# Kernel optimization log

Measured on AMD Instinct MI355X. Metric: run time of the kernel, lower is better.

## Reference

```python
import jax, jax.numpy as jnp
import numpy as np

B, N, D, NHOP = 16, 1024, 128, 4


def setup_inputs() -> dict:
    key = jax.random.key(0)
    ks = jax.random.split(key, 7)
    x = jax.random.normal(ks[0], (B, N, D), jnp.float32)
    # sparse symmetric binary adjacency with self loops (adj>0 masking semantics)
    a = (jax.random.uniform(ks[1], (B, N, N)) < 0.05).astype(jnp.float32)
    adj = jnp.maximum(a, a.transpose(0, 2, 1))
    adj = jnp.maximum(adj, jnp.eye(N, dtype=jnp.float32))
    s = 1.0 / np.sqrt(D)
    W_w = jax.random.normal(ks[2], (D, D), jnp.float32) * s
    W_b = jax.random.normal(ks[3], (D,), jnp.float32) * 0.01
    A = jax.random.normal(ks[4], (D, D), jnp.float32) * s
    gate_w = jax.random.normal(ks[5], (1, 2 * D), jnp.float32) * (1.0 / np.sqrt(2 * D))
    gate_b = jax.random.normal(ks[6], (1,), jnp.float32) * 0.01
    return {"x": x, "adj": adj, "W_w": W_w, "W_b": W_b, "A": A,
            "gate_w": gate_w, "gate_b": gate_b}


def reference(x, adj, W_w, W_b, A, gate_w, gate_b):
    # h = W(x)                                  [B,N,D]
    h = jnp.einsum('bnf,df->bnd', x, W_w) + W_b
    # bilinear attention scores e_ij = (hA)_i . h_j, symmetrized
    hA = jnp.einsum('bnd,de->bne', h, A)        # [B,N,D]
    e = jnp.einsum('bjl,bkl->bjk', hA, h)       # [B,N,N]
    e = e + e.transpose(0, 2, 1)
    att = jnp.where(adj > 0, e, jnp.zeros((), e.dtype))
    att = jax.nn.softmax(att, axis=1)           # softmax over dim=1 as in torch
    att = att * adj
    z = h
    for _ in range(NHOP):
        az = jax.nn.relu(jnp.einsum('bij,bjk->bik', att, z))   # [B,N,D]
        g_in = jnp.concatenate([x, az], axis=-1)               # [B,N,2D]
        coeff = jax.nn.sigmoid(jnp.einsum('bnf,of->bno', g_in, gate_w) + gate_b)  # [B,N,1]
        z = coeff * x + (1.0 - coeff) * az
    return z
```

## Files before the change

kernel.cpp:

```cpp
#include <hip/hip_runtime.h>
#include <cstdint>
#include <cstddef>

#define BB 16
#define NN 1024
#define DD 128
#define RR (BB*NN)
#define MAXDEG 256
#define NHOP 4

typedef unsigned long long u64;
typedef unsigned short u16;
typedef unsigned int u32;

__global__ void k_compact(const float* __restrict__ adj,
                          u64* __restrict__ bm, u32* __restrict__ deg) {
  int row = blockIdx.x;
  int l = threadIdx.x;
  const float* arow = adj + (size_t)row * NN;
  int base = 0;
  for (int r = 0; r < 16; ++r) {
    float v = arow[r * 64 + l];
    u64 m = __ballot(v > 0.0f);
    if (l == 0) bm[row * 16 + r] = m;
    base += __popcll(m);
  }
  if (l == 0) deg[row] = (u32)base;
}

__global__ void k_transpose(const float* __restrict__ A, float* __restrict__ At) {
  int e = blockIdx.x * 256 + threadIdx.x;
  int r = e >> 7, c = e & 127;
  At[c * 128 + r] = A[r * 128 + c];
}

#define GB_BK 64
__global__ __launch_bounds__(256, 3)
void k_gemm_bt(const float* __restrict__ Am, const float* __restrict__ Bm,
               const float* __restrict__ bias, float* __restrict__ Cm) {
  __shared__ float a_lds[64][GB_BK + 1];
  __shared__ float b_lds[128][GB_BK + 1];
  int t = threadIdx.x;
  int tj = t >> 5;
  int tk = t & 31;
  int rowbase = blockIdx.x * 64;
  float acc[8][4];
#pragma unroll
  for (int i = 0; i < 8; i++)
#pragma unroll
    for (int j = 0; j < 4; j++) acc[i][j] = 0.f;

  for (int kc = 0; kc < 128; kc += GB_BK) {
#pragma unroll
    for (int i = 0; i < 4; ++i) {
      int e = t + i * 256;
      int r = e >> 4, kq = e & 15;
      float4 v = *(const float4*)(Am + (size_t)(rowbase + r) * DD + kc + kq * 4);
      a_lds[r][kq * 4 + 0] = v.x; a_lds[r][kq * 4 + 1] = v.y;
      a_lds[r][kq * 4 + 2] = v.z; a_lds[r][kq * 4 + 3] = v.w;
    }
#pragma unroll
    for (int i = 0; i < 8; ++i) {
      int e = t + i * 256;
      int r = e >> 4, kq = e & 15;
      float4 v = *(const float4*)(Bm + (size_t)r * DD + kc + kq * 4);
      b_lds[r][kq * 4 + 0] = v.x; b_lds[r][kq * 4 + 1] = v.y;
      b_lds[r][kq * 4 + 2] = v.z; b_lds[r][kq * 4 + 3] = v.w;
    }
    __syncthreads();
#pragma unroll
    for (int kk = 0; kk < GB_BK; ++kk) {
      float av[8], bv[4];
#pragma unroll
      for (int i = 0; i < 8; i++) av[i] = a_lds[tj + 8 * i][kk];
#pragma unroll
      for (int j = 0; j < 4; j++) bv[j] = b_lds[tk + 32 * j][kk];
#pragma unroll
      for (int i = 0; i < 8; i++)
#pragma unroll
        for (int j = 0; j < 4; j++)
          acc[i][j] = fmaf(av[i], bv[j], acc[i][j]);
    }
    __syncthreads();
  }
#pragma unroll
  for (int i = 0; i < 8; i++) {
    int gr = rowbase + tj + 8 * i;
#pragma unroll
    for (int j = 0; j < 4; j++) {
      int c = tk + 32 * j;
      float v = acc[i][j];
      if (bias) v += bias[c];
      Cm[(size_t)gr * DD + c] = v;
    }
  }
}

#define EB_BK 32
__global__ __launch_bounds__(256, 2)
void k_e(const float* __restrict__ h, const float* __restrict__ hA,
         const u64* __restrict__ bm, float* __restrict__ ep) {
  extern __shared__ float smem[];
  float* haj = smem;
  float* hj  = smem + 128 * 33;
  float* hak = smem + 2 * 128 * 33;
  float* hk  = smem + 3 * 128 * 33;

  int pid = blockIdx.x;
  int b = blockIdx.y;
  int Jt = 0;
  while (pid >= 8 - Jt) { pid -= (8 - Jt); Jt++; }
  int Kt = Jt + pid;

  int t = threadIdx.x;
  int tj = t >> 4;
  int tk = t & 15;
  const float* hb  = h  + (size_t)b * NN * DD;
  const float* hAb = hA + (size_t)b * NN * DD;

  float acc[8][8];
#pragma unroll
  for (int i = 0; i < 8; i++)
#pragma unroll
    for (int j = 0; j < 8; j++) acc[i][j] = 0.f;

  for (int kc = 0; kc < 128; kc += EB_BK) {
#pragma unroll
    for (int i = 0; i < 4; ++i) {
      int e = t + i * 256;
      int r = e >> 3, kq = e & 7;
      float4 v;
      v = *(const float4*)(hAb + (size_t)(Jt * 128 + r) * DD + kc + kq * 4);
      haj[r * 33 + kq * 4 + 0] = v.x; haj[r * 33 + kq * 4 + 1] = v.y;
      haj[r * 33 + kq * 4 + 2] = v.z; haj[r * 33 + kq * 4 + 3] = v.w;
      v = *(const float4*)(hb + (size_t)(Jt * 128 + r) * DD + kc + kq * 4);
      hj[r * 33 + kq * 4 + 0] = v.x; hj[r * 33 + kq * 4 + 1] = v.y;
      hj[r * 33 + kq * 4 + 2] = v.z; hj[r * 33 + kq * 4 + 3] = v.w;
      v = *(const float4*)(hAb + (size_t)(Kt * 128 + r) * DD + kc + kq * 4);
      hak[r * 33 + kq * 4 + 0] = v.x; hak[r * 33 + kq * 4 + 1] = v.y;
      hak[r * 33 + kq * 4 + 2] = v.z; hak[r * 33 + kq * 4 + 3] = v.w;
      v = *(const float4*)(hb + (size_t)(Kt * 128 + r) * DD + kc + kq * 4);
      hk[r * 33 + kq * 4 + 0] = v.x; hk[r * 33 + kq * 4 + 1] = v.y;
      hk[r * 33 + kq * 4 + 2] = v.z; hk[r * 33 + kq * 4 + 3] = v.w;
    }
    __syncthreads();
#pragma unroll
    for (int kk = 0; kk < EB_BK; ++kk) {
      float aJ[8], bK[8], aK[8], bJ[8];
#pragma unroll
      for (int i = 0; i < 8; i++) { aJ[i] = haj[(tj + 16 * i) * 33 + kk]; bJ[i] = hj[(tj + 16 * i) * 33 + kk]; }
#pragma unroll
      for (int j = 0; j < 8; j++) { bK[j] = hk[(tk + 16 * j) * 33 + kk]; aK[j] = hak[(tk + 16 * j) * 33 + kk]; }
#pragma unroll
      for (int i = 0; i < 8; i++)
#pragma unroll
        for (int j = 0; j < 8; j++)
          acc[i][j] = fmaf(aJ[i], bK[j], fmaf(aK[j], bJ[i], acc[i][j]));
    }
    __syncthreads();
  }

#pragma unroll
  for (int i = 0; i < 8; i++) {
    int jr = Jt * 128 + tj + 16 * i;
    u64 w0 = bm[((size_t)b * NN + jr) * 16 + 2 * Kt];
    u64 w1 = bm[((size_t)b * NN + jr) * 16 + 2 * Kt + 1];
#pragma unroll
    for (int j = 0; j < 8; j++) {
      int kc2 = tk + 16 * j;
      int kcg = Kt * 128 + kc2;
      u64 w = (kc2 < 64) ? w0 : w1;
      int bit = (int)((w >> (kc2 & 63)) & 1ull);
      float v = bit ? acc[i][j] : 0.f;
      ep[((size_t)b * NN + jr) * NN + kcg] = v;
      ep[((size_t)b * NN + kcg) * NN + jr] = v;
    }
  }
}

__global__ void k_stats(const float* __restrict__ ep,
                        float* __restrict__ mrow, float* __restrict__ rden) {
  int row = blockIdx.x * 4 + (threadIdx.x >> 6);
  int l = threadIdx.x & 63;
  const float* er = ep + (size_t)row * NN;
  float v[16];
  float mx = -INFINITY;
#pragma unroll
  for (int r = 0; r < 16; r++) { v[r] = er[r * 64 + l]; mx = fmaxf(mx, v[r]); }
#pragma unroll
  for (int s = 1; s < 64; s <<= 1) mx = fmaxf(mx, __shfl_xor(mx, s, 64));
  float sum = 0.f;
#pragma unroll
  for (int r = 0; r < 16; r++) sum += __expf(v[r] - mx);
#pragma unroll
  for (int s = 1; s < 64; s <<= 1) sum += __shfl_xor(sum, s, 64);
  if (l == 0) { mrow[row] = mx; rden[row] = 1.0f / sum; }
}

__global__ void k_att(const float* __restrict__ ep, const u64* __restrict__ bm,
                      const float* __restrict__ mrow, const float* __restrict__ rden,
                      float* __restrict__ attv, u16* __restrict__ idx) {
  int row = blockIdx.x * 4 + (threadIdx.x >> 6);
  int l = threadIdx.x & 63;
  int bbase = row & ~(NN - 1);
  const float* er = ep + (size_t)row * NN;
  float* av = attv + (size_t)row * MAXDEG;
  u16* ir = idx + (size_t)row * MAXDEG;
  int base = 0;
  for (int r = 0; r < 16; r++) {
    u64 w = bm[row * 16 + r];
    int k = r * 64 + l;
    float v = er[k];
    if ((w >> l) & 1ull) {
      float a = __expf(v - mrow[bbase + k]) * rden[bbase + k];
      int pos = base + __popcll(w & ((1ull << l) - 1ull));
      if (pos < MAXDEG) { av[pos] = a; ir[pos] = (u16)k; }
    }
    base += __popcll(w);
  }
}

__global__ __launch_bounds__(256, 1)
void k_az(const float* __restrict__ z, const float* __restrict__ attv,
          const u16* __restrict__ idx, const u32* __restrict__ deg,
          float* __restrict__ az) {
  extern __shared__ float zl[];
  int b = blockIdx.x, kt = blockIdx.y, rc = blockIdx.z;
  int c0 = kt * 32;
  int t = threadIdx.x;
  const float* zb = z + (size_t)b * NN * DD;
#pragma unroll 8
  for (int i = 0; i < 32; i++) {
    int e = t + i * 256;
    int q = e >> 3, cq = e & 7;
    float4 v = *(const float4*)(zb + (size_t)q * DD + c0 + cq * 4);
    *(float4*)(zl + q * 36 + cq * 4) = v;
  }
  __syncthreads();

  int grow = b * NN + rc * 256 + t;
  int dgi = (int)deg[grow]; if (dgi > MAXDEG) dgi = MAXDEG;
  const u16* ir = idx + (size_t)grow * MAXDEG;
  const float* ar = attv + (size_t)grow * MAXDEG;

  float acc[32];
#pragma unroll
  for (int c = 0; c < 32; c++) acc[c] = 0.f;

  int s = 0;
  ushort4 q4 = {0, 0, 0, 0};
  float4 a4 = {0.f, 0.f, 0.f, 0.f};
  if (s + 4 <= dgi) { q4 = *(const ushort4*)(ir); a4 = *(const float4*)(ar); }
  for (; s + 4 <= dgi; s += 4) {
    ushort4 cq = q4; float4 ca = a4;
    if (s + 8 <= dgi) { q4 = *(const ushort4*)(ir + s + 4); a4 = *(const float4*)(ar + s + 4); }
    const unsigned short qq[4] = {cq.x, cq.y, cq.z, cq.w};
    const float aa[4] = {ca.x, ca.y, ca.z, ca.w};
#pragma unroll
    for (int e = 0; e < 4; e++) {
      const float* zr = zl + (int)qq[e] * 36;
      float a = aa[e];
#pragma unroll
      for (int cc = 0; cc < 8; cc++) {
        float4 zv = *(const float4*)(zr + cc * 4);
        acc[cc * 4 + 0] = fmaf(a, zv.x, acc[cc * 4 + 0]);
        acc[cc * 4 + 1] = fmaf(a, zv.y, acc[cc * 4 + 1]);
        acc[cc * 4 + 2] = fmaf(a, zv.z, acc[cc * 4 + 2]);
        acc[cc * 4 + 3] = fmaf(a, zv.w, acc[cc * 4 + 3]);
      }
    }
  }
  for (; s < dgi; s++) {
    int q = ir[s];
    float a = ar[s];
    const float* zr = zl + q * 36;
#pragma unroll
    for (int cc = 0; cc < 8; cc++) {
      float4 zv = *(const float4*)(zr + cc * 4);
      acc[cc * 4 + 0] = fmaf(a, zv.x, acc[cc * 4 + 0]);
      acc[cc * 4 + 1] = fmaf(a, zv.y, acc[cc * 4 + 1]);
      acc[cc * 4 + 2] = fmaf(a, zv.z, acc[cc * 4 + 2]);
      acc[cc * 4 + 3] = fmaf(a, zv.w, acc[cc * 4 + 3]);
    }
  }

  float* ao = az + (size_t)grow * DD + c0;
#pragma unroll
  for (int c = 0; c < 32; c += 4) {
    float4 v;
    v.x = fmaxf(acc[c + 0], 0.f); v.y = fmaxf(acc[c + 1], 0.f);
    v.z = fmaxf(acc[c + 2], 0.f); v.w = fmaxf(acc[c + 3], 0.f);
    *(float4*)(ao + c) = v;
  }
}

__global__ void k_gate(const float* __restrict__ x, const float* __restrict__ az,
                       const float* __restrict__ gw, const float* __restrict__ gb,
                       float* __restrict__ zo) {
  int row = blockIdx.x * 4 + (threadIdx.x >> 6);
  int l = threadIdx.x & 63;
  const float* xr = x + (size_t)row * DD;
  const float* ar = az + (size_t)row * DD;
  float x0 = xr[l], x1 = xr[l + 64];
  float a0 = ar[l], a1 = ar[l + 64];
  float p = gw[l] * x0 + gw[l + 64] * x1 + gw[128 + l] * a0 + gw[192 + l] * a1;
#pragma unroll
  for (int s = 1; s < 64; s <<= 1) p += __shfl_xor(p, s, 64);
  float cf = 1.0f / (1.0f + __expf(-(p + gb[0])));
  zo[(size_t)row * DD + l] = cf * x0 + (1.f - cf) * a0;
  zo[(size_t)row * DD + l + 64] = cf * x1 + (1.f - cf) * a1;
}

extern "C" void kernel_launch(void* const* d_in, const int* in_sizes, int n_in,
                              void* d_out, int out_size, void* d_ws, size_t ws_size,
                              hipStream_t stream) {
  const float* x   = (const float*)d_in[0];
  const float* adj = (const float*)d_in[1];
  const float* W_w = (const float*)d_in[2];
  const float* W_b = (const float*)d_in[3];
  const float* A   = (const float*)d_in[4];
  const float* gw  = (const float*)d_in[5];
  const float* gb  = (const float*)d_in[6];
  float* out = (float*)d_out;

  char* p = (char*)d_ws;
  auto alloc = [&](size_t bytes) -> void* {
    void* r = (void*)p;
    p += (bytes + 255) & ~(size_t)255;
    return r;
  };
  float* h    = (float*)alloc((size_t)RR * DD * 4);
  float* hA   = (float*)alloc((size_t)RR * DD * 4);
  float* ep   = (float*)alloc((size_t)RR * NN * 4);
  u64*   bm   = (u64*)alloc((size_t)RR * 16 * 8);
  u32*   deg  = (u32*)alloc((size_t)RR * 4);
  float* mrow = (float*)alloc((size_t)RR * 4);
  float* rden = (float*)alloc((size_t)RR * 4);
  float* attv = (float*)alloc((size_t)RR * MAXDEG * 4);
  u16*   idx  = (u16*)alloc((size_t)RR * MAXDEG * 2);
  float* At   = (float*)alloc((size_t)DD * DD * 4);

  k_compact<<<RR, 64, 0, stream>>>(adj, bm, deg);
  k_transpose<<<64, 256, 0, stream>>>(A, At);
  k_gemm_bt<<<RR / 64, 256, 0, stream>>>(x, W_w, W_b, h);
  k_gemm_bt<<<RR / 64, 256, 0, stream>>>(h, At, nullptr, hA);
  size_t e_lds = (size_t)4 * 128 * 33 * sizeof(float);
  k_e<<<dim3(36, 16), 256, e_lds, stream>>>(h, hA, bm, ep);
  k_stats<<<RR / 4, 256, 0, stream>>>(ep, mrow, rden);
  k_att<<<RR / 4, 256, 0, stream>>>(ep, bm, mrow, rden, attv, idx);

  size_t az_lds = (size_t)1024 * 36 * sizeof(float);
  for (int hop = 0; hop < NHOP; ++hop) {
    k_az<<<dim3(16, 4, 4), 256, az_lds, stream>>>(h, attv, idx, deg, hA);
    float* zo = (hop == NHOP - 1) ? out : h;
    k_gate<<<RR / 4, 256, 0, stream>>>(x, hA, gw, gb, zo);
  }
}
```

Measured before the change: 501.9 us.

## Replace sparse gather aggregation with dense split-bf16 MFMA matmul per hop

Drops the compacted sparse attention list (values plus indices) and instead writes a dense attention matrix split into bf16 hi/lo halves. z is likewise transposed and split into hi/lo bf16. Each hop then runs a 3-term bf16 MFMA GEMM with K-split partial sums, reduced inside a new fused gate kernel that also emits the next hop's transposed bf16 z. The k_e tile is also reshaped to a smaller K block, static LDS and higher occupancy. Dense compute on a ~5% sparse matrix does much more raw work and the hi/lo split gives near-fp32 accuracy only approximately; the bet is that MFMA throughput outweighs the scalar LDS gather.

New measurement: 490.9 us. 1.02x faster.

```diff
diff --git a/kernel.cpp b/kernel.cpp
--- a/kernel.cpp
+++ b/kernel.cpp
@@ -6,26 +6,34 @@
 #define NN 1024
 #define DD 128
 #define RR (BB*NN)
-#define MAXDEG 256
 #define NHOP 4
+#define KSPLIT 4
 
 typedef unsigned long long u64;
 typedef unsigned short u16;
 typedef unsigned int u32;
-
-__global__ void k_compact(const float* __restrict__ adj,
-                          u64* __restrict__ bm, u32* __restrict__ deg) {
+typedef __attribute__((ext_vector_type(8))) short bf16x8;
+typedef __attribute__((ext_vector_type(4))) float f32x4;
+
+__device__ __forceinline__ u16 f2bf(float f) {
+  union { float f; u32 u; } c; c.f = f;
+  u32 r = c.u + 0x7FFFu + ((c.u >> 16) & 1u);
+  return (u16)(r >> 16);
+}
+__device__ __forceinline__ float bf2f(u16 h) {
+  union { u32 u; float f; } c; c.u = ((u32)h) << 16;
+  return c.f;
+}
+
+__global__ void k_compact(const float* __restrict__ adj, u64* __restrict__ bm) {
   int row = blockIdx.x;
   int l = threadIdx.x;
   const float* arow = adj + (size_t)row * NN;
-  int base = 0;
   for (int r = 0; r < 16; ++r) {
     float v = arow[r * 64 + l];
     u64 m = __ballot(v > 0.0f);
     if (l == 0) bm[row * 16 + r] = m;
-    base += __popcll(m);
-  }
-  if (l == 0) deg[row] = (u32)base;
+  }
 }
 
 __global__ void k_transpose(const float* __restrict__ A, float* __restrict__ At) {
@@ -41,8 +49,7 @@
   __shared__ float a_lds[64][GB_BK + 1];
   __shared__ float b_lds[128][GB_BK + 1];
   int t = threadIdx.x;
-  int tj = t >> 5;
-  int tk = t & 31;
+  int tj = t >> 5, tk = t & 31;
   int rowbase = blockIdx.x * 64;
   float acc[8][4];
 #pragma unroll
@@ -96,15 +103,16 @@
   }
 }
 
-#define EB_BK 32
-__global__ __launch_bounds__(256, 2)
+#define EB_BK 16
+#define EP 20
+__global__ __launch_bounds__(256, 3)
 void k_e(const float* __restrict__ h, const float* __restrict__ hA,
          const u64* __restrict__ bm, float* __restrict__ ep) {
-  extern __shared__ float smem[];
+  __shared__ float smem[4 * 128 * EP];
   float* haj = smem;
-  float* hj  = smem + 128 * 33;
-  float* hak = smem + 2 * 128 * 33;
-  float* hk  = smem + 3 * 128 * 33;
+  float* hj  = smem + 128 * EP;
+  float* hak = smem + 2 * 128 * EP;
+  float* hk  = smem + 3 * 128 * EP;
 
   int pid = blockIdx.x;
   int b = blockIdx.y;
@@ -113,10 +121,11 @@
   int Kt = Jt + pid;
 
   int t = threadIdx.x;
-  int tj = t >> 4;
-  int tk = t & 15;
+  int tj = t >> 4, tk = t & 15;
   const float* hb  = h  + (size_t)b * NN * DD;
   const float* hAb = hA + (size_t)b * NN * DD;
+  const float* srcs[4] = { hAb + (size_t)Jt * 128 * DD, hb + (size_t)Jt * 128 * DD,
+                           hAb + (size_t)Kt * 128 * DD, hb + (size_t)Kt * 128 * DD };
 
   float acc[8][8];
 #pragma unroll
@@ -126,36 +135,37 @@
 
   for (int kc = 0; kc < 128; kc += EB_BK) {
 #pragma unroll
-    for (int i = 0; i < 4; ++i) {
-      int e = t + i * 256;
-      int r = e >> 3, kq = e & 7;
-      float4 v;
-      v = *(const float4*)(hAb + (size_t)(Jt * 128 + r) * DD + kc + kq * 4);
-      haj[r * 33 + kq * 4 + 0] = v.x; haj[r * 33 + kq * 4 + 1] = v.y;
-      haj[r * 33 + kq * 4 + 2] = v.z; haj[r * 33 + kq * 4 + 3] = v.w;
-      v = *(const float4*)(hb + (size_t)(Jt * 128 + r) * DD + kc + kq * 4);
-      hj[r * 33 + kq * 4 + 0] = v.x; hj[r * 33 + kq * 4 + 1] = v.y;
-      hj[r * 33 + kq * 4 + 2] = v.z; hj[r * 33 + kq * 4 + 3] = v.w;
-      v = *(const float4*)(hAb + (size_t)(Kt * 128 + r) * DD + kc + kq * 4);
-      hak[r * 33 + kq * 4 + 0] = v.x; hak[r * 33 + kq * 4 + 1] = v.y;
-      hak[r * 33 + kq * 4 + 2] = v.z; hak[r * 33 + kq * 4 + 3] = v.w;
-      v = *(const float4*)(hb + (size_t)(Kt * 128 + r) * DD + kc + kq * 4);
-      hk[r * 33 + kq * 4 + 0] = v.x; hk[r * 33 + kq * 4 + 1] = v.y;
-      hk[r * 33 + kq * 4 + 2] = v.z; hk[r * 33 + kq * 4 + 3] = v.w;
-    }
-    __syncthreads();
-#pragma unroll
-    for (int kk = 0; kk < EB_BK; ++kk) {
-      float aJ[8], bK[8], aK[8], bJ[8];
-#pragma unroll
-      for (int i = 0; i < 8; i++) { aJ[i] = haj[(tj + 16 * i) * 33 + kk]; bJ[i] = hj[(tj + 16 * i) * 33 + kk]; }
-#pragma unroll
-      for (int j = 0; j < 8; j++) { bK[j] = hk[(tk + 16 * j) * 33 + kk]; aK[j] = hak[(tk + 16 * j) * 33 + kk]; }
+    for (int arr = 0; arr < 4; ++arr) {
+      const float* sp = srcs[arr];
+      float* dp = smem + arr * 128 * EP;
+#pragma unroll
+      for (int i = 0; i < 2; ++i) {
+        int e = t + i * 256;
+        int r = e >> 2, kq = e & 3;
+        float4 v = *(const float4*)(sp + (size_t)r * DD + kc + kq * 4);
+        *(float4*)(dp + r * EP + kq * 4) = v;
+      }
+    }
+    __syncthreads();
+#pragma unroll
+    for (int kk = 0; kk < EB_BK; kk += 2) {
+      float2 aJ[8], bJ[8], aK[8], bK[8];
+#pragma unroll
+      for (int i = 0; i < 8; ++i) {
+        aJ[i] = *(const float2*)(haj + (tj + 16 * i) * EP + kk);
+        bJ[i] = *(const float2*)(hj  + (tj + 16 * i) * EP + kk);
+        aK[i] = *(const float2*)(hak + (tk + 16 * i) * EP + kk);
+        bK[i] = *(const float2*)(hk  + (tk + 16 * i) * EP + kk);
+      }
 #pragma unroll
       for (int i = 0; i < 8; i++)
 #pragma unroll
-        for (int j = 0; j < 8; j++)
-          acc[i][j] = fmaf(aJ[i], bK[j], fmaf(aK[j], bJ[i], acc[i][j]));
+        for (int j = 0; j < 8; j++) {
+          acc[i][j] = fmaf(aJ[i].x, bK[j].x, acc[i][j]);
+          acc[i][j] = fmaf(aJ[i].y, bK[j].y, acc[i][j]);
+          acc[i][j] = fmaf(aK[j].x, bJ[i].x, acc[i][j]);
+          acc[i][j] = fmaf(aK[j].y, bJ[i].y, acc[i][j]);
+        }
     }
     __syncthreads();
   }
@@ -197,118 +207,246 @@
   if (l == 0) { mrow[row] = mx; rden[row] = 1.0f / sum; }
 }
 
-__global__ void k_att(const float* __restrict__ ep, const u64* __restrict__ bm,
-                      const float* __restrict__ mrow, const float* __restrict__ rden,
-                      float* __restrict__ attv, u16* __restrict__ idx) {
-  int row = blockIdx.x * 4 + (threadIdx.x >> 6);
-  int l = threadIdx.x & 63;
-  int bbase = row & ~(NN - 1);
-  const float* er = ep + (size_t)row * NN;
-  float* av = attv + (size_t)row * MAXDEG;
-  u16* ir = idx + (size_t)row * MAXDEG;
-  int base = 0;
-  for (int r = 0; r < 16; r++) {
-    u64 w = bm[row * 16 + r];
-    int k = r * 64 + l;
-    float v = er[k];
-    if ((w >> l) & 1ull) {
-      float a = __expf(v - mrow[bbase + k]) * rden[bbase + k];
-      int pos = base + __popcll(w & ((1ull << l) - 1ull));
-      if (pos < MAXDEG) { av[pos] = a; ir[pos] = (u16)k; }
-    }
-    base += __popcll(w);
+__global__ __launch_bounds__(256, 2)
+void k_att_dense(const float* __restrict__ ep, const u64* __restrict__ bm,
+                 const float* __restrict__ mrow, const float* __restrict__ rden,
+                 u16* __restrict__ ahi, u16* __restrict__ alo) {
+  __shared__ float ml[NN];
+  __shared__ float rl[NN];
+  int g = blockIdx.x;
+  int b = g >> 4;
+  int t = threadIdx.x;
+  int w = t >> 6, l = t & 63;
+#pragma unroll
+  for (int i = 0; i < 4; ++i) {
+    ml[t + i * 256] = mrow[(size_t)b * NN + t + i * 256];
+    rl[t + i * 256] = rden[(size_t)b * NN + t + i * 256];
+  }
+  __syncthreads();
+
+  for (int rr = 0; rr < 16; ++rr) {
+    int row = g * 64 + rr * 4 + w;
+    const float* er = ep + (size_t)row * NN;
+    u16* oh = ahi + (size_t)row * NN;
+    u16* ol = alo + (size_t)row * NN;
+    const u64* bw = bm + (size_t)row * 16;
+#pragma unroll
+    for (int pass = 0; pass < 4; ++pass) {
+      int c = pass * 256 + l * 4;
+      float4 e4 = *(const float4*)(er + c);
+      u64 wbits = bw[c >> 6];
+      float av[4];
+#pragma unroll
+      for (int j = 0; j < 4; ++j) {
+        int k = c + j;
+        float e = (j == 0) ? e4.x : (j == 1) ? e4.y : (j == 2) ? e4.z : e4.w;
+        int bit = (int)((wbits >> (k & 63)) & 1ull);
+        av[j] = bit ? __expf(e - ml[k]) * rl[k] : 0.f;
+      }
+      ushort4 vh, vl;
+      vh.x = f2bf(av[0]); vl.x = f2bf(av[0] - bf2f(vh.x));
+      vh.y = f2bf(av[1]); vl.y = f2bf(av[1] - bf2f(vh.y));
+      vh.z = f2bf(av[2]); vl.z = f2bf(av[2] - bf2f(vh.z));
+      vh.w = f2bf(av[3]); vl.w = f2bf(av[3] - bf2f(vh.w));
+      *(ushort4*)(oh + c) = vh;
+      *(ushort4*)(ol + c) = vl;
+    }
+  }
+}
+
+#define TP 133
+__global__ __launch_bounds__(256, 2)
+void k_prep(const float* __restrict__ h, u16* __restrict__ zth, u16* __restrict__ ztl) {
+  __shared__ float tile[64 * TP];
+  int g = blockIdx.x;
+  int b = g >> 4;
+  int rbb = (g & 15) * 64;
+  int t = threadIdx.x;
+#pragma unroll
+  for (int i = 0; i < 8; ++i) {
+    int e = t + i * 256;
+    int r = e >> 5, cq = e & 31;
+    float4 v = *(const float4*)(h + (size_t)(g * 64 + r) * DD + cq * 4);
+    tile[r * TP + cq * 4 + 0] = v.x; tile[r * TP + cq * 4 + 1] = v.y;
+    tile[r * TP + cq * 4 + 2] = v.z; tile[r * TP + cq * 4 + 3] = v.w;
+  }
+  __syncthreads();
+#pragma unroll
+  for (int it = 0; it < 32; ++it) {
+    int c = it * 4 + (t >> 6);
+    int row = t & 63;
+    float v = tile[row * TP + c];
+    u16 hi = f2bf(v);
+    u16 lo = f2bf(v - bf2f(hi));
+    size_t o = (size_t)b * DD * NN + (size_t)c * NN + rbb + row;
+    zth[o] = hi; ztl[o] = lo;
   }
 }
 
 __global__ __launch_bounds__(256, 1)
-void k_az(const float* __restrict__ z, const float* __restrict__ attv,
-          const u16* __restrict__ idx, const u32* __restrict__ deg,
-          float* __restrict__ az) {
-  extern __shared__ float zl[];
-  int b = blockIdx.x, kt = blockIdx.y, rc = blockIdx.z;
-  int c0 = kt * 32;
-  int t = threadIdx.x;
-  const float* zb = z + (size_t)b * NN * DD;
-#pragma unroll 8
-  for (int i = 0; i < 32; i++) {
+void k_az_mfma(const u16* __restrict__ ahi, const u16* __restrict__ alo,
+               const u16* __restrict__ zth, const u16* __restrict__ ztl,
+               float* __restrict__ azp) {
+  __shared__ u16 lds[4][128 * 64];
+  int rt = blockIdx.x;
+  int ks = blockIdx.y;
+  int b  = blockIdx.z;
+  int t = threadIdx.x;
+  int w = t >> 6, l = t & 63;
+  int wm = w >> 1, wn = w & 1;
+  int k0 = ks * (NN / KSPLIT);
+
+  const u16* srcs[4] = {
+    ahi + ((size_t)b * NN + rt * 128) * NN + k0,
+    alo + ((size_t)b * NN + rt * 128) * NN + k0,
+    zth + (size_t)b * DD * NN + k0,
+    ztl + (size_t)b * DD * NN + k0
+  };
+
+  f32x4 acc[4][4];
+#pragma unroll
+  for (int i = 0; i < 4; i++)
+#pragma unroll
+    for (int j = 0; j < 4; j++) acc[i][j] = (f32x4)(0.f);
+
+  for (int kb = 0; kb < NN / KSPLIT; kb += 64) {
+#pragma unroll
+    for (int arr = 0; arr < 4; ++arr) {
+      const u16* sp = srcs[arr] + kb;
+#pragma unroll
+      for (int c = 0; c < 4; ++c) {
+        int chunk = w * 4 + c;
+        int row = chunk * 8 + (l >> 3);
+        int slot = l & 7;
+        const u16* gp = sp + (size_t)row * NN + ((slot ^ (row & 7)) << 3);
+        u16* lp = &lds[arr][chunk * 512];
+        __builtin_amdgcn_global_load_lds(
+            (const __attribute__((address_space(1))) void*)gp,
+            (__attribute__((address_space(3))) void*)lp, 16, 0, 0);
+      }
+    }
+    __syncthreads();
+
+#pragma unroll
+    for (int ks2 = 0; ks2 < 2; ++ks2) {
+      int s = ks2 * 4 + (l >> 4);
+      bf16x8 ah[4], al4[4], bh[4], bl4[4];
+#pragma unroll
+      for (int mi = 0; mi < 4; ++mi) {
+        int m = wm * 64 + mi * 16 + (l & 15);
+        int off = m * 64 + ((s ^ (m & 7)) << 3);
+        ah[mi]  = *(const bf16x8*)&lds[0][off];
+        al4[mi] = *(const bf16x8*)&lds[1][off];
+      }
+#pragma unroll
+      for (int ni = 0; ni < 4; ++ni) {
+        int n = wn * 64 + ni * 16 + (l & 15);
+        int off = n * 64 + ((s ^ (n & 7)) << 3);
+        bh[ni]  = *(const bf16x8*)&lds[2][off];
+        bl4[ni] = *(const bf16x8*)&lds[3][off];
+      }
+#pragma unroll
+      for (int mi = 0; mi < 4; ++mi)
+#pragma unroll
+        for (int ni = 0; ni < 4; ++ni) {
+          acc[mi][ni] = __builtin_amdgcn_mfma_f32_16x16x32_bf16(ah[mi],  bh[ni],  acc[mi][ni], 0, 0, 0);
+          acc[mi][ni] = __builtin_amdgcn_mfma_f32_16x16x32_bf16(ah[mi],  bl4[ni], acc[mi][ni], 0, 0, 0);
+          acc[mi][ni] = __builtin_amdgcn_mfma_f32_16x16x32_bf16(al4[mi], bh[ni],  acc[mi][ni], 0, 0, 0);
+        }
+    }
+    __syncthreads();
+  }
+
+  float* dst = azp + ((size_t)ks * RR + (size_t)b * NN + rt * 128) * DD;
+#pragma unroll
+  for (int mi = 0; mi < 4; ++mi)
+#pragma unroll
+    for (int ni = 0; ni < 4; ++ni) {
+      int row = wm * 64 + mi * 16 + ((l >> 4) << 2);
+      int col = wn * 64 + ni * 16 + (l & 15);
+#pragma unroll
+      for (int r = 0; r < 4; ++r)
+        dst[(size_t)(row + r) * DD + col] = acc[mi][ni][r];
+    }
+}
+
+__global__ __launch_bounds__(256, 2)
+void k_gate2(const float* __restrict__ x, const float* __restrict__ azp,
+             const float* __restrict__ gw, const float* __restrict__ gb, int last,
+             u16* __restrict__ zth, u16* __restrict__ ztl, float* __restrict__ out) {
+  __shared__ float axl[64 * TP];
+  __shared__ float coeff[64];
+  int g = blockIdx.x;
+  int b = g >> 4;
+  int rbb = (g & 15) * 64;
+  int t = threadIdx.x;
+
+#pragma unroll
+  for (int i = 0; i < 8; ++i) {
     int e = t + i * 256;
-    int q = e >> 3, cq = e & 7;
-    float4 v = *(const float4*)(zb + (size_t)q * DD + c0 + cq * 4);
-    *(float4*)(zl + q * 36 + cq * 4) = v;
+    int r = e >> 5, cq = e & 31;
+    size_t o = (size_t)(g * 64 + r) * DD + cq * 4;
+    float4 v0 = *(const float4*)(azp + o);
+    float4 v1 = *(const float4*)(azp + (size_t)RR * DD + o);
+    float4 v2 = *(const float4*)(azp + 2 * (size_t)RR * DD + o);
+    float4 v3 = *(const float4*)(azp + 3 * (size_t)RR * DD + o);
+    axl[r * TP + cq * 4 + 0] = fmaxf(v0.x + v1.x + v2.x + v3.x, 0.f);
+    axl[r * TP + cq * 4 + 1] = fmaxf(v0.y + v1.y + v2.y + v3.y, 0.f);
+    axl[r * TP + cq * 4 + 2] = fmaxf(v0.z + v1.z + v2.z + v3.z, 0.f);
+    axl[r * TP + cq * 4 + 3] = fmaxf(v0.w + v1.w + v2.w + v3.w, 0.f);
   }
   __syncthreads();
 
-  int grow = b * NN + rc * 256 + t;
-  int dgi = (int)deg[grow]; if (dgi > MAXDEG) dgi = MAXDEG;
-  const u16* ir = idx + (size_t)grow * MAXDEG;
-  const float* ar = attv + (size_t)grow * MAXDEG;
-
-  float acc[32];
-#pragma unroll
-  for (int c = 0; c < 32; c++) acc[c] = 0.f;
-
-  int s = 0;
-  ushort4 q4 = {0, 0, 0, 0};
-  float4 a4 = {0.f, 0.f, 0.f, 0.f};
-  if (s + 4 <= dgi) { q4 = *(const ushort4*)(ir); a4 = *(const float4*)(ar); }
-  for (; s + 4 <= dgi; s += 4) {
-    ushort4 cq = q4; float4 ca = a4;
-    if (s + 8 <= dgi) { q4 = *(const ushort4*)(ir + s + 4); a4 = *(const float4*)(ar + s + 4); }
-    const unsigned short qq[4] = {cq.x, cq.y, cq.z, cq.w};
-    const float aa[4] = {ca.x, ca.y, ca.z, ca.w};
-#pragma unroll
-    for (int e = 0; e < 4; e++) {
-      const float* zr = zl + (int)qq[e] * 36;
-      float a = aa[e];
-#pragma unroll
-      for (int cc = 0; cc < 8; cc++) {
-        float4 zv = *(const float4*)(zr + cc * 4);
-        acc[cc * 4 + 0] = fmaf(a, zv.x, acc[cc * 4 + 0]);
-        acc[cc * 4 + 1] = fmaf(a, zv.y, acc[cc * 4 + 1]);
-        acc[cc * 4 + 2] = fmaf(a, zv.z, acc[cc * 4 + 2]);
-        acc[cc * 4 + 3] = fmaf(a, zv.w, acc[cc * 4 + 3]);
-      }
-    }
-  }
-  for (; s < dgi; s++) {
-    int q = ir[s];
-    float a = ar[s];
-    const float* zr = zl + q * 36;
-#pragma unroll
-    for (int cc = 0; cc < 8; cc++) {
-      float4 zv = *(const float4*)(zr + cc * 4);
-      acc[cc * 4 + 0] = fmaf(a, zv.x, acc[cc * 4 + 0]);
-      acc[cc * 4 + 1] = fmaf(a, zv.y, acc[cc * 4 + 1]);
-      acc[cc * 4 + 2] = fmaf(a, zv.z, acc[cc * 4 + 2]);
-      acc[cc * 4 + 3] = fmaf(a, zv.w, acc[cc * 4 + 3]);
-    }
-  }
-
-  float* ao = az + (size_t)grow * DD + c0;
-#pragma unroll
-  for (int c = 0; c < 32; c += 4) {
-    float4 v;
-    v.x = fmaxf(acc[c + 0], 0.f); v.y = fmaxf(acc[c + 1], 0.f);
-    v.z = fmaxf(acc[c + 2], 0.f); v.w = fmaxf(acc[c + 3], 0.f);
-    *(float4*)(ao + c) = v;
-  }
-}
-
-__global__ void k_gate(const float* __restrict__ x, const float* __restrict__ az,
-                       const float* __restrict__ gw, const float* __restrict__ gb,
-                       float* __restrict__ zo) {
-  int row = blockIdx.x * 4 + (threadIdx.x >> 6);
-  int l = threadIdx.x & 63;
-  const float* xr = x + (size_t)row * DD;
-  const float* ar = az + (size_t)row * DD;
-  float x0 = xr[l], x1 = xr[l + 64];
-  float a0 = ar[l], a1 = ar[l + 64];
-  float p = gw[l] * x0 + gw[l + 64] * x1 + gw[128 + l] * a0 + gw[192 + l] * a1;
-#pragma unroll
-  for (int s = 1; s < 64; s <<= 1) p += __shfl_xor(p, s, 64);
-  float cf = 1.0f / (1.0f + __expf(-(p + gb[0])));
-  zo[(size_t)row * DD + l] = cf * x0 + (1.f - cf) * a0;
-  zo[(size_t)row * DD + l + 64] = cf * x1 + (1.f - cf) * a1;
+  {
+    int rl = t >> 2, part = t & 3;
+    const float* xr = x + (size_t)(g * 64 + rl) * DD;
+    float s = 0.f;
+#pragma unroll
+    for (int i = 0; i < 32; ++i) {
+      int c = part * 32 + i;
+      s += gw[c] * xr[c] + gw[128 + c] * axl[rl * TP + c];
+    }
+    s += __shfl_xor(s, 1, 64);
+    s += __shfl_xor(s, 2, 64);
+    if (part == 0) coeff[rl] = 1.0f / (1.0f + __expf(-(s + gb[0])));
+  }
+  __syncthreads();
+
+#pragma unroll
+  for (int i = 0; i < 8; ++i) {
+    int e = t + i * 256;
+    int r = e >> 5, cq = e & 31;
+    float cf = coeff[r];
+    float4 xv = *(const float4*)(x + (size_t)(g * 64 + r) * DD + cq * 4);
+    axl[r * TP + cq * 4 + 0] = cf * xv.x + (1.f - cf) * axl[r * TP + cq * 4 + 0];
+    axl[r * TP + cq * 4 + 1] = cf * xv.y + (1.f - cf) * axl[r * TP + cq * 4 + 1];
+    axl[r * TP + cq * 4 + 2] = cf * xv.z + (1.f - cf) * axl[r * TP + cq * 4 + 2];
+    axl[r * TP + cq * 4 + 3] = cf * xv.w + (1.f - cf) * axl[r * TP + cq * 4 + 3];
+  }
+  __syncthreads();
+
+  if (last) {
+#pragma unroll
+    for (int i = 0; i < 8; ++i) {
+      int e = t + i * 256;
+      int r = e >> 5, cq = e & 31;
+      float4 v;
+      v.x = axl[r * TP + cq * 4 + 0]; v.y = axl[r * TP + cq * 4 + 1];
+      v.z = axl[r * TP + cq * 4 + 2]; v.w = axl[r * TP + cq * 4 + 3];
+      *(float4*)(out + (size_t)(g * 64 + r) * DD + cq * 4) = v;
+    }
+  } else {
+#pragma unroll
+    for (int it = 0; it < 32; ++it) {
+      int c = it * 4 + (t >> 6);
+      int row = t & 63;
+      float v = axl[row * TP + c];
+      u16 hi = f2bf(v);
+      u16 lo = f2bf(v - bf2f(hi));
+      size_t o = (size_t)b * DD * NN + (size_t)c * NN + rbb + row;
+      zth[o] = hi; ztl[o] = lo;
+    }
+  }
 }
 
 extern "C" void kernel_launch(void* const* d_in, const int* in_sizes, int n_in,
@@ -333,26 +471,28 @@
   float* hA   = (float*)alloc((size_t)RR * DD * 4);
   float* ep   = (float*)alloc((size_t)RR * NN * 4);
   u64*   bm   = (u64*)alloc((size_t)RR * 16 * 8);
-  u32*   deg  = (u32*)alloc((size_t)RR * 4);
   float* mrow = (float*)alloc((size_t)RR * 4);
   float* rden = (float*)alloc((size_t)RR * 4);
-  float* attv = (float*)alloc((size_t)RR * MAXDEG * 4);
-  u16*   idx  = (u16*)alloc((size_t)RR * MAXDEG * 2);
+  u16*   ahi  = (u16*)alloc((size_t)RR * NN * 2);
+  u16*   alo  = (u16*)alloc((size_t)RR * NN * 2);
   float* At   = (float*)alloc((size_t)DD * DD * 4);
 
-  k_compact<<<RR, 64, 0, stream>>>(adj, bm, deg);
+  float* azp = ep;
+  u16* zth = (u16*)((char*)ep + ((size_t)40 << 20));
+  u16* ztl = (u16*)((char*)ep + ((size_t)48 << 20));
+
+  k_compact<<<RR, 64, 0, stream>>>(adj, bm);
   k_transpose<<<64, 256, 0, stream>>>(A, At);
   k_gemm_bt<<<RR / 64, 256, 0, stream>>>(x, W_w, W_b, h);
   k_gemm_bt<<<RR / 64, 256, 0, stream>>>(h, At, nullptr, hA);
-  size_t e_lds = (size_t)4 * 128 * 33 * sizeof(float);
-  k_e<<<dim3(36, 16), 256, e_lds, stream>>>(h, hA, bm, ep);
+  k_e<<<dim3(36, BB), 256, 0, stream>>>(h, hA, bm, ep);
   k_stats<<<RR / 4, 256, 0, stream>>>(ep, mrow, rden);
-  k_att<<<RR / 4, 256, 0, stream>>>(ep, bm, mrow, rden, attv, idx);
-
-  size_t az_lds = (size_t)1024 * 36 * sizeof(float);
+  k_att_dense<<<RR / 64, 256, 0, stream>>>(ep, bm, mrow, rden, ahi, alo);
+  k_prep<<<RR / 64, 256, 0, stream>>>(h, zth, ztl);
+
   for (int hop = 0; hop < NHOP; ++hop) {
-    k_az<<<dim3(16, 4, 4), 256, az_lds, stream>>>(h, attv, idx, deg, hA);
-    float* zo = (hop == NHOP - 1) ? out : h;
-    k_gate<<<RR / 4, 256, 0, stream>>>(x, hA, gw, gb, zo);
-  }
-}
+    k_az_mfma<<<dim3(8, KSPLIT, BB), 256, 0, stream>>>(ahi, alo, zth, ztl, azp);
+    int last = (hop == NHOP - 1);
+    k_gate2<<<RR / 64, 256, 0, stream>>>(x, azp, gw, gb, last, zth, ztl, out);
+  }
+}
```
